# Optimization experiments

Measured on AMD Instinct MI355X. Metric: run time of the kernel, lower is better.

Reference implementation:

```python
import jax, jax.numpy as jnp
import numpy as np

K = 3  # kernel size
PAD = 1  # padding (stride=1, dilation=1)


def _unfold(x, k=K, pad=PAD):
    """im2col: x [B,C,H,W] -> [B,C,k,k,H,W] (stride=1, dilation=1)."""
    B, C, H, W = x.shape
    xp = jnp.pad(x, ((0, 0), (0, 0), (pad, pad), (pad, pad)))
    # small fixed k*k loop, stacked into window dims
    rows = []
    for i in range(k):
        cols = [xp[:, :, i:i + H, j:j + W] for j in range(k)]
        rows.append(jnp.stack(cols, axis=2))  # [B,C,k,H,W]
    return jnp.stack(rows, axis=2)  # [B,C,k,k,H,W]


def setup_inputs() -> dict:
    key = jax.random.key(0)
    k1, k2, k3, k4 = jax.random.split(key, 4)
    B, C, O, H, W = 4, 64, 64, 128, 128
    inputs = jax.random.normal(k1, (B, C, H, W), dtype=jnp.float32)
    alpha = jax.random.uniform(k2, (B, 1, H, W), dtype=jnp.float32)
    fan_in = C * K * K
    weight = jax.random.normal(k3, (O, C, K, K), dtype=jnp.float32) / np.sqrt(fan_in)
    bias = jax.random.normal(k4, (O,), dtype=jnp.float32) / np.sqrt(fan_in)
    return {
        "inputs": inputs,
        "alpha": alpha,
        "weight": weight,
        "bias": bias,
        "a": jnp.float32(-4.0),
        "b": jnp.float32(4.0),
        "c": jnp.float32(1.0),
    }


def reference(inputs, alpha, weight, bias, a, b, c):
    # spatially-varying kernel from alpha: (a*x + b)*x + c on unfolded windows
    alpha_wins = _unfold(alpha)                      # [B,1,k,k,H,W]
    kernel = (a * alpha_wins + b) * alpha_wins + c   # [B,1,k,k,H,W]
    inputs_wins = _unfold(inputs)                    # [B,C,k,k,H,W]
    inputs_mul_kernel = inputs_wins * kernel         # broadcast over C
    out = jnp.einsum('ijklmn,ojkl->iomn', inputs_mul_kernel, weight)
    out = out + bias[None, :, None, None]
    return out
```

## Files before the change

kernel.cpp:

```cpp
#include <hip/hip_runtime.h>

typedef __bf16 bf16x8 __attribute__((ext_vector_type(8)));
typedef float f32x4 __attribute__((ext_vector_type(4)));

#define BB 4
#define CC 64
#define OO 64
#define HH 128
#define WW 128

__global__ __launch_bounds__(256) void prep_kernel(
    const float* __restrict__ in, const float* __restrict__ alpha,
    const float* __restrict__ w,
    const float* __restrict__ pa, const float* __restrict__ pb, const float* __restrict__ pc,
    unsigned short* __restrict__ xs, unsigned short* __restrict__ aw)
{
    __shared__ float trans[64][132];
    int tid = threadIdx.x;

    if (blockIdx.x >= 512) {
        int gid = (blockIdx.x - 512) * 256 + tid;
        if (gid >= 4608) return;
        int og  = gid / 1152;
        int rem = gid - og * 1152;
        int t = rem >> 6;
        int l = rem & 63;
        int q = l >> 4;
        int m = l & 15;
        int o  = og * 16 + m;
        int ij = t >> 1;
        int ch = t & 1;
        int i = ij / 3;
        int j = ij - i * 3;
        union { unsigned short u[8]; uint4 v; } pk;
#pragma unroll
        for (int jj = 0; jj < 8; ++jj) {
            int c = ch * 32 + q * 8 + jj;
            float wf = w[((o * CC + c) * 3 + i) * 3 + j];
            __bf16 h = (__bf16)wf;
            pk.u[jj] = __builtin_bit_cast(unsigned short, h);
        }
        ((uint4*)aw)[gid] = pk.v;
        return;
    }

    int bid = blockIdx.x;
    int y   = bid & 127;
    int b   = bid >> 7;

    int x16 = tid & 31;
    int c8  = tid >> 5;
    const float* src = in + ((size_t)(b * CC) * HH + y) * WW;
#pragma unroll
    for (int k = 0; k < 8; ++k) {
        int c = c8 * 8 + k;
        float4 v = *(const float4*)(src + (size_t)c * HH * WW + x16 * 4);
        *(float4*)(&trans[c][x16 * 4]) = v;
    }
    __syncthreads();

    int xw = tid >> 1;
    int cg = tid & 1;
    float A  = *pa, Bc = *pb, Cc = *pc;
    float av = alpha[(b * HH + y) * WW + xw];
    float f  = (A * av + Bc) * av + Cc;
    union { unsigned short u[32]; uint4 v4[4]; } pk;
#pragma unroll
    for (int k = 0; k < 32; ++k) {
        __bf16 h = (__bf16)(trans[cg * 32 + k][xw] * f);
        pk.u[k] = __builtin_bit_cast(unsigned short, h);
    }
    uint4* dst = (uint4*)(xs + (((size_t)(b * HH + y) * WW + xw) * CC + cg * 32));
    dst[0] = pk.v4[0];
    dst[1] = pk.v4[1];
    dst[2] = pk.v4[2];
    dst[3] = pk.v4[3];
}

__global__ __launch_bounds__(256, 2) void conv_kernel(
    const unsigned short* __restrict__ xs, const unsigned short* __restrict__ aw,
    const float* __restrict__ bias, float* __restrict__ out)
{
    __shared__ unsigned short tile[3 * 130 * 72];

    int n   = blockIdx.x;
    int xcd = n & 7;
    int idx = n >> 3;
    int b   = xcd >> 1;
    int y   = (xcd & 1) * 64 + idx;
    int tid = threadIdx.x;

    for (int s = tid; s < 3120; s += 256) {
        int g  = s & 7;
        int rx = s >> 3;
        int r  = rx / 130;
        int xt = rx - r * 130;
        int yy = y + r - 1;
        int xg = xt - 1;
        uint4 val = make_uint4(0u, 0u, 0u, 0u);
        if ((unsigned)yy < (unsigned)HH && (unsigned)xg < (unsigned)WW)
            val = *(const uint4*)(xs + (((size_t)(b * HH + yy) * WW + xg) * CC + g * 8));
        *(uint4*)(tile + (r * 130 + xt) * 72 + g * 8) = val;
    }
    __syncthreads();

    int wv = tid >> 6;
    int l  = tid & 63;
    int oh = wv & 1;
    int nh = wv >> 1;
    int q  = l >> 4;
    int m  = l & 15;

    f32x4 acc[2][4];
#pragma unroll
    for (int ag = 0; ag < 2; ++ag)
#pragma unroll
        for (int nf = 0; nf < 4; ++nf)
            acc[ag][nf] = (f32x4){0.f, 0.f, 0.f, 0.f};

    const uint4* awv = (const uint4*)aw + (size_t)(oh * 2) * 18 * 64 + l;

#pragma unroll 3
    for (int ij = 0; ij < 9; ++ij) {
        const int i = ij / 3;
        const int j = ij - i * 3;
#pragma unroll
        for (int ch = 0; ch < 2; ++ch) {
            const int t = ij * 2 + ch;
            bf16x8 afrag[2], bfrag[4];
#pragma unroll
            for (int ag = 0; ag < 2; ++ag)
                afrag[ag] = __builtin_bit_cast(bf16x8, awv[(ag * 18 + t) * 64]);
#pragma unroll
            for (int nf = 0; nf < 4; ++nf) {
                int xt = nh * 64 + nf * 16 + m + j;
                bfrag[nf] = __builtin_bit_cast(bf16x8,
                    *(const uint4*)(tile + (i * 130 + xt) * 72 + ch * 32 + q * 8));
            }
#pragma unroll
            for (int ag = 0; ag < 2; ++ag)
#pragma unroll
                for (int nf = 0; nf < 4; ++nf)
                    acc[ag][nf] = __builtin_amdgcn_mfma_f32_16x16x32_bf16(
                        afrag[ag], bfrag[nf], acc[ag][nf], 0, 0, 0);
        }
    }

#pragma unroll
    for (int ag = 0; ag < 2; ++ag) {
#pragma unroll
        for (int r = 0; r < 4; ++r) {
            int o = (oh * 2 + ag) * 16 + q * 4 + r;
            float bv = bias[o];
#pragma unroll
            for (int nf = 0; nf < 4; ++nf) {
                int x = nh * 64 + nf * 16 + m;
                out[((size_t)(b * OO + o) * HH + y) * WW + x] = acc[ag][nf][r] + bv;
            }
        }
    }
}

extern "C" void kernel_launch(void* const* d_in, const int* in_sizes, int n_in,
                              void* d_out, int out_size, void* d_ws, size_t ws_size,
                              hipStream_t stream) {
    const float* inputs = (const float*)d_in[0];
    const float* alpha  = (const float*)d_in[1];
    const float* weight = (const float*)d_in[2];
    const float* bias   = (const float*)d_in[3];
    const float* pa     = (const float*)d_in[4];
    const float* pb     = (const float*)d_in[5];
    const float* pc     = (const float*)d_in[6];
    float* out = (float*)d_out;

    unsigned short* aw = (unsigned short*)d_ws;
    unsigned short* xs = (unsigned short*)((char*)d_ws + 131072);

    prep_kernel<<<512 + 18, 256, 0, stream>>>(inputs, alpha, weight, pa, pb, pc, xs, aw);
    conv_kernel<<<BB * HH, 256, 0, stream>>>(xs, aw, bias, out);
}
```

Measured before the change: 95.10 us.

## Pre-pad activations in workspace and stage tiles via direct global-to-LDS loads

The prep kernel now writes the bf16 activations into a zero-padded [B,130,130,64] layout, which removes the bounds checks in the conv kernel. The conv kernel fills its LDS tile with global_load_lds (direct global-to-LDS DMA) instead of loading through registers. It replaces the padded 72-element row stride with an XOR-style swizzle of the 16-byte chunks so the MFMA B-fragment reads avoid bank conflicts. In exchange, prep does extra writes for the halo, the workspace is slightly larger, and the swizzle indexing must match exactly between the load and read sides.

```diff
diff --git a/kernel.cpp b/kernel.cpp
--- a/kernel.cpp
+++ b/kernel.cpp
@@ -8,6 +8,11 @@
 #define OO 64
 #define HH 128
 #define WW 128
+
+#define ROWCH (130 * 8)
+
+typedef __attribute__((address_space(1))) const void GASV;
+typedef __attribute__((address_space(3))) void LASV;
 
 __global__ __launch_bounds__(256) void prep_kernel(
     const float* __restrict__ in, const float* __restrict__ alpha,
@@ -47,6 +52,19 @@
     int bid = blockIdx.x;
     int y   = bid & 127;
     int b   = bid >> 7;
+    uint4* xsv = (uint4*)xs;
+
+    if (tid < 16) {
+        size_t rowbase = (size_t)(b * 130 + y + 1) * ROWCH;
+        int xt = (tid < 8) ? 0 : 129;
+        int g  = tid & 7;
+        xsv[rowbase + (size_t)xt * 8 + g] = make_uint4(0u, 0u, 0u, 0u);
+    }
+    if (y == 0 || y == 127) {
+        size_t zbase = (size_t)(b * 130 + (y == 0 ? 0 : 129)) * ROWCH;
+        for (int s = tid; s < ROWCH; s += 256)
+            xsv[zbase + s] = make_uint4(0u, 0u, 0u, 0u);
+    }
 
     int x16 = tid & 31;
     int c8  = tid >> 5;
@@ -70,7 +88,7 @@
         __bf16 h = (__bf16)(trans[cg * 32 + k][xw] * f);
         pk.u[k] = __builtin_bit_cast(unsigned short, h);
     }
-    uint4* dst = (uint4*)(xs + (((size_t)(b * HH + y) * WW + xw) * CC + cg * 32));
+    uint4* dst = xsv + (size_t)(b * 130 + y + 1) * ROWCH + (size_t)(xw + 1) * 8 + cg * 4;
     dst[0] = pk.v4[0];
     dst[1] = pk.v4[1];
     dst[2] = pk.v4[2];
@@ -81,7 +99,8 @@
     const unsigned short* __restrict__ xs, const unsigned short* __restrict__ aw,
     const float* __restrict__ bias, float* __restrict__ out)
 {
-    __shared__ unsigned short tile[3 * 130 * 72];
+    __shared__ uint4 tile4[3120];
+    unsigned short* tile = (unsigned short*)tile4;
 
     int n   = blockIdx.x;
     int xcd = n & 7;
@@ -89,23 +108,26 @@
     int b   = xcd >> 1;
     int y   = (xcd & 1) * 64 + idx;
     int tid = threadIdx.x;
-
-    for (int s = tid; s < 3120; s += 256) {
-        int g  = s & 7;
-        int rx = s >> 3;
-        int r  = rx / 130;
-        int xt = rx - r * 130;
-        int yy = y + r - 1;
-        int xg = xt - 1;
-        uint4 val = make_uint4(0u, 0u, 0u, 0u);
-        if ((unsigned)yy < (unsigned)HH && (unsigned)xg < (unsigned)WW)
-            val = *(const uint4*)(xs + (((size_t)(b * HH + yy) * WW + xg) * CC + g * 8));
-        *(uint4*)(tile + (r * 130 + xt) * 72 + g * 8) = val;
+    int wv  = tid >> 6;
+    int l   = tid & 63;
+
+    const uint4* win = (const uint4*)xs + (size_t)(b * 130 + y) * ROWCH;
+
+#pragma unroll
+    for (int it = 0; it < 13; ++it) {
+        int s_lin = it * 256 + tid;
+        if (s_lin < 3120) {
+            int rx = s_lin >> 3;
+            int s  = s_lin & 7;
+            int xt = rx % 130;
+            int wch = (s - xt) & 7;
+            const uint4* gp = win + rx * 8 + wch;
+            LASV* lp = (LASV*)(tile4 + it * 256 + wv * 64);
+            __builtin_amdgcn_global_load_lds((GASV*)gp, lp, 16, 0, 0);
+        }
     }
     __syncthreads();
 
-    int wv = tid >> 6;
-    int l  = tid & 63;
     int oh = wv & 1;
     int nh = wv >> 1;
     int q  = l >> 4;
@@ -127,6 +149,7 @@
 #pragma unroll
         for (int ch = 0; ch < 2; ++ch) {
             const int t = ij * 2 + ch;
+            const int w = ch * 4 + q;
             bf16x8 afrag[2], bfrag[4];
 #pragma unroll
             for (int ag = 0; ag < 2; ++ag)
@@ -134,8 +157,9 @@
 #pragma unroll
             for (int nf = 0; nf < 4; ++nf) {
                 int xt = nh * 64 + nf * 16 + m + j;
+                int sl = (w + xt) & 7;
                 bfrag[nf] = __builtin_bit_cast(bf16x8,
-                    *(const uint4*)(tile + (i * 130 + xt) * 72 + ch * 32 + q * 8));
+                    *(const uint4*)(tile + ((i * 130 + xt) * 8 + sl) * 8));
             }
 #pragma unroll
             for (int ag = 0; ag < 2; ++ag)
```

After: 95.18 us. No clear change (+0.1%).
